# Kernel optimization log

Hardware: AMD Instinct MI355X
Metric: run time of the kernel (lower is better)

The kernel has to match this reference:

```python
import jax, jax.numpy as jnp
import numpy as np

N_HEADS = 16
EMBED = 1024
T = 2048        # given tokens
CACHE_NUM = 1024  # prepended cache tokens (x[0,-1] in the original)


def setup_inputs() -> dict:
    key = jax.random.key(0)
    k1, k2 = jax.random.split(key)
    qkv = jax.random.normal(k1, (T, 3 * EMBED), dtype=jnp.float32)
    # In the original these cache rows are torch.randn generated inside forward;
    # we lift them into a deterministic explicit input with identical semantics.
    cache = jax.random.normal(k2, (CACHE_NUM, 3 * EMBED), dtype=jnp.float32)
    return {"qkv": qkv, "cache": cache}


def reference(qkv, cache):
    C = EMBED
    H = N_HEADS
    D = C // H  # head_dim = 64
    t = qkv.shape[0]
    tc = cache.shape[0]
    t_full = t + tc  # T_ in the original

    gq, gk, gv = jnp.split(qkv, 3, axis=1)      # each [T, C]
    cq, ck, cv = jnp.split(cache, 3, axis=1)    # each [cache_num, C]

    q = jnp.concatenate([cq, gq], axis=0)  # [T_, C]
    k = jnp.concatenate([ck, gk], axis=0)
    v = jnp.concatenate([cv, gv], axis=0)

    # [T_, C] -> [H, T_, D]
    q = q.reshape(t_full, H, D).transpose(1, 0, 2)
    k = k.reshape(t_full, H, D).transpose(1, 0, 2)
    v = v.reshape(t_full, H, D).transpose(1, 0, 2)

    scale = 1.0 / np.sqrt(D).astype(np.float32)
    att = jnp.einsum('htd,hsd->hts', q, k) * scale  # [H, T_, T_]

    causal = jnp.tril(jnp.ones((t_full, t_full), dtype=bool))
    att = jnp.where(causal[None, :, :], att, jnp.float32(-jnp.inf))
    att = jax.nn.softmax(att, axis=-1)
    # attn_dropout is identity in eval / p=0

    y = jnp.einsum('hts,hsd->htd', att, v)          # [H, T_, D]
    y = y.transpose(1, 0, 2).reshape(t_full, C)     # [T_, C]
    return y[tc:, :]                                # drop cache rows -> [T, C]
```

## Files before the change

### kernel.cpp

```cpp
#include <hip/hip_runtime.h>
#include <cmath>


typedef _Float16 f16;
typedef __attribute__((ext_vector_type(8))) _Float16 f16x8;
typedef __attribute__((ext_vector_type(4))) _Float16 f16x4;
typedef __attribute__((ext_vector_type(2))) _Float16 f16x2;
typedef __attribute__((ext_vector_type(4))) float    f32x4;

constexpr int TC  = 1024;
constexpr int C3  = 3072;
constexpr int CE  = 1024;
constexpr int NH  = 16;
constexpr int TQ  = 2048;
constexpr int NKT = 48;

constexpr size_t KV_ELEMS = (size_t)NH * NKT * 4096;

constexpr int SPLITS[16] = {2,2,3,3,3,3,4,4,4,4,5,5,5,5,6,6};
constexpr int PRE[16]    = {0,2,4,7,10,13,16,20,24,28,32,37,42,47,52,58};
constexpr int NSLOT      = 64;

constexpr size_t OPART_E = (size_t)NSLOT * NH * 128 * 64;
constexpr size_t LPART_F = (size_t)NSLOT * NH * 128;

__device__ __forceinline__ void dma16(const void* g, void* l) {
    __builtin_amdgcn_global_load_lds(
        (const __attribute__((address_space(1))) void*)g,
        (__attribute__((address_space(3))) void*)l, 16, 0, 0);
}

__device__ __forceinline__ f16x2 pkrtz(float a, float b) {
    return __builtin_bit_cast(f16x2, __builtin_amdgcn_cvt_pkrtz(a, b));
}

__device__ __forceinline__ float fexp2(float x) {
    return __builtin_amdgcn_exp2f(x);
}

__global__ __launch_bounds__(256)
void prepass_f16(const float* __restrict__ qkv, const float* __restrict__ cache,
                 f16* __restrict__ Kt, f16* __restrict__ Vt)
{
    const int b   = blockIdx.x;
    const int xcd = b & 7;
    const int j   = b >> 3;
    const int h   = xcd * 2 + ((j >= 48) ? 1 : 0);
    const int kt  = (j >= 48) ? (j - 48) : j;

    const int tid = threadIdx.x;
    const int bt  = kt * 64;
    const float* src = (bt < TC) ? (cache + (size_t)bt * C3)
                                 : (qkv + (size_t)(bt - TC) * C3);
    f16* ktile = Kt + (size_t)(h * NKT + kt) * 4096;
    f16* vtile = Vt + (size_t)(h * NKT + kt) * 4096;

    __shared__ f16 vtmp[64 * 66];

    {
        const int tok = tid >> 2;
        const int c4  = tid & 3;
        const float* p = src + (size_t)tok * C3 + h * 64 + CE + c4 * 16;
        f32x4 x0 = ((const f32x4*)p)[0], x1 = ((const f32x4*)p)[1];
        f32x4 x2 = ((const f32x4*)p)[2], x3 = ((const f32x4*)p)[3];
        const int ch0 = (2 * c4)     ^ (tok & 7);
        const int ch1 = (2 * c4 + 1) ^ (tok & 7);
        *(f16x8*)&ktile[tok * 64 + ch0 * 8] =
            (f16x8){(f16)x0.x,(f16)x0.y,(f16)x0.z,(f16)x0.w,
                    (f16)x1.x,(f16)x1.y,(f16)x1.z,(f16)x1.w};
        *(f16x8*)&ktile[tok * 64 + ch1 * 8] =
            (f16x8){(f16)x2.x,(f16)x2.y,(f16)x2.z,(f16)x2.w,
                    (f16)x3.x,(f16)x3.y,(f16)x3.z,(f16)x3.w};
    }
    {
        const int tok  = tid >> 2;
        const int dblk = (tid & 3) * 16;
        const float* p = src + (size_t)tok * C3 + h * 64 + 2 * CE + dblk;
        f32x4 x0 = ((const f32x4*)p)[0], x1 = ((const f32x4*)p)[1];
        f32x4 x2 = ((const f32x4*)p)[2], x3 = ((const f32x4*)p)[3];
        float v[16] = {x0.x,x0.y,x0.z,x0.w, x1.x,x1.y,x1.z,x1.w,
                       x2.x,x2.y,x2.z,x2.w, x3.x,x3.y,x3.z,x3.w};
        f16* dst = &vtmp[tok * 66 + dblk];
        #pragma unroll
        for (int i = 0; i < 8; ++i)
            *(f16x2*)&dst[2 * i] = (f16x2){(f16)v[2 * i], (f16)v[2 * i + 1]};
    }
    __syncthreads();
    {
        const int d  = tid >> 2;
        const int oq = tid & 3;
        const int qd = oq ^ (d & 3);
        const int d4 = (d >> 2) & 1;
        f16 col[16];
        #pragma unroll
        for (int e = 0; e < 2; ++e)
            #pragma unroll
            for (int bb = 0; bb < 2; ++bb) {
                const int t0 = ((e ^ d4) * 2 + bb) * 16 + qd * 4;
                #pragma unroll
                for (int j = 0; j < 4; ++j)
                    col[e * 8 + bb * 4 + j] = vtmp[(t0 + j) * 66 + d];
            }
        *(f16x8*)&vtile[d * 64 + oq * 16] =
            (f16x8){col[0],col[1],col[2],col[3],col[4],col[5],col[6],col[7]};
        *(f16x8*)&vtile[d * 64 + oq * 16 + 8] =
            (f16x8){col[8],col[9],col[10],col[11],col[12],col[13],col[14],col[15]};
    }
}

__device__ __forceinline__ void tile_loop(
    const char* kg, const char* vg, int t0, int t1, int qbase_w,
    int l15, int quad, int ksw, int soff,
    const f16x8 (&qfrag)[2][2], f16 (&sKV)[2][8192],
    f32x4 (&o_accT)[2][4], float (&l_i)[2])
{
    {
        char* kl = (char*)&sKV[0][0]    + soff;
        char* vl = (char*)&sKV[0][4096] + soff;
        dma16(kg, kl);           dma16(kg + 1024, kl + 1024);
        dma16(vg, vl);           dma16(vg + 1024, vl + 1024);
    }
    int cur = 0;

    const int sA = ((quad ^ (l15 & 3)) << 1) + ((l15 >> 2) & 1);

    for (int kt = t0; kt < t1; ++kt) {
        asm volatile("s_waitcnt vmcnt(0) lgkmcnt(0)" ::: "memory");
        __syncthreads();

        kg += 8192; vg += 8192;
        if (kt + 1 < t1) {
            char* kl = (char*)&sKV[cur ^ 1][0]    + soff;
            char* vl = (char*)&sKV[cur ^ 1][4096] + soff;
            dma16(kg, kl);       dma16(kg + 1024, kl + 1024);
            dma16(vg, vl);       dma16(vg + 1024, vl + 1024);
        }
        const f16* sK  = &sKV[cur][0];
        const f16* sVT = &sKV[cur][4096];
        cur ^= 1;

        f32x4 sacc[2][4];
        #pragma unroll
        for (int u = 0; u < 2; ++u)
            #pragma unroll
            for (int kb = 0; kb < 4; ++kb) sacc[u][kb] = (f32x4){0.f,0.f,0.f,0.f};
        #pragma unroll
        for (int kb = 0; kb < 4; ++kb) {
            const int ib = (kb * 16 + l15) * 64 + ksw;
            f16x8 a0 = *(const f16x8*)&sK[ib];
            f16x8 a1 = *(const f16x8*)&sK[ib ^ 32];
            #pragma unroll
            for (int u = 0; u < 2; ++u) {
                sacc[u][kb] = __builtin_amdgcn_mfma_f32_16x16x32_f16(a0, qfrag[u][0], sacc[u][kb], 0, 0, 0);
                sacc[u][kb] = __builtin_amdgcn_mfma_f32_16x16x32_f16(a1, qfrag[u][1], sacc[u][kb], 0, 0, 0);
            }
        }

        if (kt * 64 + 63 > qbase_w) {
            #pragma unroll
            for (int u = 0; u < 2; ++u) {
                const int qg = qbase_w + u * 16 + l15;
                #pragma unroll
                for (int kb = 0; kb < 4; ++kb) {
                    const int kq = kt * 64 + kb * 16 + quad * 4;
                    #pragma unroll
                    for (int r = 0; r < 4; ++r)
                        if (kq + r > qg) sacc[u][kb][r] = -INFINITY;
                }
            }
        }

        f16x4 pfrag[2][4];
        #pragma unroll
        for (int u = 0; u < 2; ++u) {
            float ls = 0.f;
            #pragma unroll
            for (int kb = 0; kb < 4; ++kb) {
                const float p0 = fexp2(sacc[u][kb][0]);
                const float p1 = fexp2(sacc[u][kb][1]);
                const float p2 = fexp2(sacc[u][kb][2]);
                const float p3 = fexp2(sacc[u][kb][3]);
                ls += (p0 + p1) + (p2 + p3);
                f16x2 lo = pkrtz(p0, p1);
                f16x2 hi = pkrtz(p2, p3);
                pfrag[u][kb] = __builtin_shufflevector(lo, hi, 0, 1, 2, 3);
            }
            l_i[u] += ls;
        }

        #pragma unroll
        for (int dblk = 0; dblk < 4; ++dblk) {
            const int row = dblk * 16 + l15;
            f16x8 vv01 = *(const f16x8*)&sVT[row * 64 + sA * 8];
            f16x8 vv23 = *(const f16x8*)&sVT[row * 64 + (sA ^ 1) * 8];
            f16x4 vf[4];
            vf[0] = __builtin_shufflevector(vv01, vv01, 0, 1, 2, 3);
            vf[1] = __builtin_shufflevector(vv01, vv01, 4, 5, 6, 7);
            vf[2] = __builtin_shufflevector(vv23, vv23, 0, 1, 2, 3);
            vf[3] = __builtin_shufflevector(vv23, vv23, 4, 5, 6, 7);
            #pragma unroll
            for (int kb = 0; kb < 4; ++kb)
                #pragma unroll
                for (int u = 0; u < 2; ++u)
                    o_accT[u][dblk] = __builtin_amdgcn_mfma_f32_16x16x16f16(
                        vf[kb], pfrag[u][kb], o_accT[u][dblk], 0, 0, 0);
        }
    }
}

__global__ __launch_bounds__(256, 4)
void attn_splitk(const float* __restrict__ qkv,
                 const f16* __restrict__ Kt,
                 const f16* __restrict__ Vt,
                 f16*  __restrict__ Opart,
                 float* __restrict__ lpart)
{
    const int bb = blockIdx.x;
    const int xcd = bb & 7;
    const int j   = bb >> 3;
    const int h   = xcd * 2 + (j >> 6);
    const int g   = j & 63;
    int qt = 0;
    #pragma unroll
    for (int i = 1; i < 16; ++i) qt += (g >= PRE[i]) ? 1 : 0;
    const int s   = g - PRE[qt];
    const int nsp = SPLITS[qt];
    const int nkt = 2 * qt + 18;
    const int t0  = nkt * s / nsp;
    const int t1  = nkt * (s + 1) / nsp;

    const int tid  = threadIdx.x;
    const int w    = tid >> 6;
    const int lane = tid & 63;
    const int l15  = lane & 15;
    const int quad = lane >> 4;

    __shared__ __align__(16) f16 sKV[2][8192];

    const float qs = 0.125f * 1.44269504088896f;
    f16x8 qfrag[2][2];
    #pragma unroll
    for (int u = 0; u < 2; ++u) {
        const float* qp = qkv + (size_t)(qt * 128 + w * 32 + u * 16 + l15) * C3
                              + h * 64 + quad * 8;
        #pragma unroll
        for (int c = 0; c < 2; ++c) {
            f32x4 a = *(const f32x4*)(qp + c * 32);
            f32x4 b = *(const f32x4*)(qp + c * 32 + 4);
            qfrag[u][c] = (f16x8){(f16)(a.x * qs), (f16)(a.y * qs),
                                  (f16)(a.z * qs), (f16)(a.w * qs),
                                  (f16)(b.x * qs), (f16)(b.y * qs),
                                  (f16)(b.z * qs), (f16)(b.w * qs)};
        }
    }

    f32x4 o_accT[2][4];
    #pragma unroll
    for (int u = 0; u < 2; ++u)
        #pragma unroll
        for (int d = 0; d < 4; ++d) o_accT[u][d] = (f32x4){0.f, 0.f, 0.f, 0.f};
    float l_i[2] = {0.f, 0.f};

    const int qbase_w = TC + qt * 128 + w * 32;
    const int soff = w * 2048 + lane * 16;
    const char* kg = (const char*)(Kt + (size_t)(h * NKT + t0) * 4096) + soff;
    const char* vg = (const char*)(Vt + (size_t)(h * NKT + t0) * 4096) + soff;
    const int ksw = (quad ^ (l15 & 7)) * 8;

    tile_loop(kg, vg, t0, t1, qbase_w, l15, quad, ksw, soff,
              qfrag, sKV, o_accT, l_i);

    #pragma unroll
    for (int u = 0; u < 2; ++u) {
        float lf = l_i[u];
        lf += __shfl_xor(lf, 16);
        lf += __shfl_xor(lf, 32);
        const int qloc = w * 32 + u * 16 + l15;
        const int slot = PRE[qt] + s;
        f16*   op = Opart + ((size_t)slot * NH + h) * (128 * 64);
        float* lp = lpart + ((size_t)slot * NH + h) * 128;
        #pragma unroll
        for (int dblk = 0; dblk < 4; ++dblk) {
            f32x4 o = o_accT[u][dblk];
            f16x2 lo = pkrtz(o.x, o.y);
            f16x2 hi = pkrtz(o.z, o.w);
            *(f16x4*)&op[qloc * 64 + dblk * 16 + quad * 4] =
                __builtin_shufflevector(lo, hi, 0, 1, 2, 3);
        }
        if (quad == 0) lp[qloc] = lf;
    }
}

__global__ __launch_bounds__(256)
void attn_direct(const float* __restrict__ qkv,
                 const f16* __restrict__ Kt,
                 const f16* __restrict__ Vt,
                 float* __restrict__ out)
{
    const int bb  = blockIdx.x;
    const int h   = bb & 15;
    const int idx = bb >> 4;
    const int qt  = (h < 8) ? idx : 15 - idx;
    const int nsp = SPLITS[qt];
    const int nkt = 2 * qt + 18;

    const int tid  = threadIdx.x;
    const int w    = tid >> 6;
    const int lane = tid & 63;
    const int l15  = lane & 15;
    const int quad = lane >> 4;

    __shared__ __align__(16) f16 sKV[2][8192];

    const float qs = 0.125f * 1.44269504088896f;
    f16x8 qfrag[2][2];
    #pragma unroll
    for (int u = 0; u < 2; ++u) {
        const float* qp = qkv + (size_t)(qt * 128 + w * 32 + u * 16 + l15) * C3
                              + h * 64 + quad * 8;
        #pragma unroll
        for (int c = 0; c < 2; ++c) {
            f32x4 a = *(const f32x4*)(qp + c * 32);
            f32x4 b = *(const f32x4*)(qp + c * 32 + 4);
            qfrag[u][c] = (f16x8){(f16)(a.x * qs), (f16)(a.y * qs),
                                  (f16)(a.z * qs), (f16)(a.w * qs),
                                  (f16)(b.x * qs), (f16)(b.y * qs),
                                  (f16)(b.z * qs), (f16)(b.w * qs)};
        }
    }

    const int qbase_w = TC + qt * 128 + w * 32;
    const int soff = w * 2048 + lane * 16;
    const char* kg0 = (const char*)(Kt + (size_t)h * NKT * 4096) + soff;
    const char* vg0 = (const char*)(Vt + (size_t)h * NKT * 4096) + soff;
    const int ksw = (quad ^ (l15 & 7)) * 8;

    f32x4 osum[2][4];
    #pragma unroll
    for (int u = 0; u < 2; ++u)
        #pragma unroll
        for (int d = 0; d < 4; ++d) osum[u][d] = (f32x4){0.f, 0.f, 0.f, 0.f};
    float lsum[2] = {0.f, 0.f};

    for (int s = 0; s < nsp; ++s) {
        if (s) __syncthreads();
        const int t0 = nkt * s / nsp;
        const int t1 = nkt * (s + 1) / nsp;

        f32x4 o_accT[2][4];
        #pragma unroll
        for (int u = 0; u < 2; ++u)
            #pragma unroll
            for (int d = 0; d < 4; ++d) o_accT[u][d] = (f32x4){0.f,0.f,0.f,0.f};
        float l_i[2] = {0.f, 0.f};

        tile_loop(kg0 + (size_t)t0 * 8192, vg0 + (size_t)t0 * 8192,
                  t0, t1, qbase_w, l15, quad, ksw, soff,
                  qfrag, sKV, o_accT, l_i);

        #pragma unroll
        for (int u = 0; u < 2; ++u) {
            float lf = l_i[u];
            lf += __shfl_xor(lf, 16);
            lf += __shfl_xor(lf, 32);
            lsum[u] += lf;
            #pragma unroll
            for (int dblk = 0; dblk < 4; ++dblk) {
                f32x4 o = o_accT[u][dblk];
                f16x2 lo = pkrtz(o.x, o.y);
                f16x2 hi = pkrtz(o.z, o.w);
                osum[u][dblk].x += (float)lo[0];
                osum[u][dblk].y += (float)lo[1];
                osum[u][dblk].z += (float)hi[0];
                osum[u][dblk].w += (float)hi[1];
            }
        }
    }

    #pragma unroll
    for (int u = 0; u < 2; ++u) {
        const float inv = 1.0f / lsum[u];
        const int qloc = w * 32 + u * 16 + l15;
        const int gq = qt * 128 + qloc;
        #pragma unroll
        for (int dblk = 0; dblk < 4; ++dblk) {
            f32x4 o = osum[u][dblk];
            *(f32x4*)&out[(size_t)gq * CE + h * 64 + dblk * 16 + quad * 4] =
                (f32x4){o.x * inv, o.y * inv, o.z * inv, o.w * inv};
        }
    }
}

__global__ __launch_bounds__(256)
void combine_splits(const f16* __restrict__ Opart,
                    const float* __restrict__ lpart,
                    float* __restrict__ out)
{
    const int t  = blockIdx.x * 256 + threadIdx.x;
    const int d4 = t & 15;
    const int q  = (t >> 4) & (TQ - 1);
    const int h  = t >> 15;

    const int qt    = q >> 7;
    const int qloc  = q & 127;
    const int nsp   = SPLITS[qt];
    const int slot0 = PRE[qt];

    float lsum = 0.f;
    f32x4 acc = (f32x4){0.f, 0.f, 0.f, 0.f};
    for (int s = 0; s < nsp; ++s) {
        const size_t sb = (size_t)(slot0 + s) * NH + h;
        lsum += lpart[sb * 128 + qloc];
        f16x4 o = *(const f16x4*)&Opart[sb * (128 * 64) + qloc * 64 + d4 * 4];
        acc.x += (float)o[0]; acc.y += (float)o[1];
        acc.z += (float)o[2]; acc.w += (float)o[3];
    }
    const float inv = 1.0f / lsum;
    *(f32x4*)&out[(size_t)q * CE + h * 64 + d4 * 4] =
        (f32x4){acc.x * inv, acc.y * inv, acc.z * inv, acc.w * inv};
}

extern "C" void kernel_launch(void* const* d_in, const int* in_sizes, int n_in,
                              void* d_out, int out_size, void* d_ws, size_t ws_size,
                              hipStream_t stream)
{
    const float* qkv   = (const float*)d_in[0];
    const float* cache = (const float*)d_in[1];
    float*       out   = (float*)d_out;
    (void)in_sizes; (void)n_in; (void)out_size;

    const size_t kv_bytes = 2 * KV_ELEMS * sizeof(f16);
    const size_t need     = kv_bytes + OPART_E * sizeof(f16)
                          + LPART_F * sizeof(float);

    f16*   Kt    = (f16*)d_ws;
    f16*   Vt    = Kt + KV_ELEMS;
    f16*   Opart = (f16*)((char*)d_ws + kv_bytes);
    float* lpart = (float*)((char*)Opart + OPART_E * sizeof(f16));

    const int split = (ws_size >= need) ? 1 : 0;

    prepass_f16<<<dim3(NH * NKT), dim3(256), 0, stream>>>(qkv, cache, Kt, Vt);
    if (split) {
        attn_splitk<<<dim3(1024), dim3(256), 0, stream>>>(qkv, Kt, Vt, Opart, lpart);
        combine_splits<<<dim3(NH * TQ * 16 / 256), dim3(256), 0, stream>>>(
            Opart, lpart, out);
    } else {
        attn_direct<<<dim3(256), dim3(256), 0, stream>>>(qkv, Kt, Vt, out);
    }
}
```

Baseline: 112.7 us.

## Fuse prepass, split-K attention and combine into one cooperative kernel

```diff
diff --git a/kernel.cpp b/kernel.cpp
--- a/kernel.cpp
+++ b/kernel.cpp
@@ -1,5 +1,8 @@
 #include <hip/hip_runtime.h>
+#include <hip/hip_cooperative_groups.h>
 #include <cmath>
+
+namespace cg = cooperative_groups;
 
 
 typedef _Float16 f16;
@@ -38,24 +41,21 @@
     return __builtin_amdgcn_exp2f(x);
 }
 
-__global__ __launch_bounds__(256)
-void prepass_f16(const float* __restrict__ qkv, const float* __restrict__ cache,
-                 f16* __restrict__ Kt, f16* __restrict__ Vt)
-{
-    const int b   = blockIdx.x;
+__device__ __forceinline__ void prepass_body(
+    int b, int tid, const float* __restrict__ qkv,
+    const float* __restrict__ cache, f16* __restrict__ Kt,
+    f16* __restrict__ Vt, f16* vtmp)
+{
     const int xcd = b & 7;
     const int j   = b >> 3;
     const int h   = xcd * 2 + ((j >= 48) ? 1 : 0);
     const int kt  = (j >= 48) ? (j - 48) : j;
 
-    const int tid = threadIdx.x;
     const int bt  = kt * 64;
     const float* src = (bt < TC) ? (cache + (size_t)bt * C3)
                                  : (qkv + (size_t)(bt - TC) * C3);
     f16* ktile = Kt + (size_t)(h * NKT + kt) * 4096;
     f16* vtile = Vt + (size_t)(h * NKT + kt) * 4096;
-
-    __shared__ f16 vtmp[64 * 66];
 
     {
         const int tok = tid >> 2;
@@ -95,11 +95,11 @@
         #pragma unroll
         for (int e = 0; e < 2; ++e)
             #pragma unroll
-            for (int bb = 0; bb < 2; ++bb) {
-                const int t0 = ((e ^ d4) * 2 + bb) * 16 + qd * 4;
+            for (int bb2 = 0; bb2 < 2; ++bb2) {
+                const int t0 = ((e ^ d4) * 2 + bb2) * 16 + qd * 4;
                 #pragma unroll
-                for (int j = 0; j < 4; ++j)
-                    col[e * 8 + bb * 4 + j] = vtmp[(t0 + j) * 66 + d];
+                for (int jj = 0; jj < 4; ++jj)
+                    col[e * 8 + bb2 * 4 + jj] = vtmp[(t0 + jj) * 66 + d];
             }
         *(f16x8*)&vtile[d * 64 + oq * 16] =
             (f16x8){col[0],col[1],col[2],col[3],col[4],col[5],col[6],col[7]};
@@ -208,14 +208,11 @@
     }
 }
 
-__global__ __launch_bounds__(256, 4)
-void attn_splitk(const float* __restrict__ qkv,
-                 const f16* __restrict__ Kt,
-                 const f16* __restrict__ Vt,
-                 f16*  __restrict__ Opart,
-                 float* __restrict__ lpart)
-{
-    const int bb = blockIdx.x;
+__device__ __forceinline__ void attn_sk_body(
+    int bb, const float* __restrict__ qkv, const f16* __restrict__ Kt,
+    const f16* __restrict__ Vt, f16* __restrict__ Opart,
+    float* __restrict__ lpart, f16 (&sKV)[2][8192])
+{
     const int xcd = bb & 7;
     const int j   = bb >> 3;
     const int h   = xcd * 2 + (j >> 6);
@@ -234,8 +231,6 @@
     const int lane = tid & 63;
     const int l15  = lane & 15;
     const int quad = lane >> 4;
-
-    __shared__ __align__(16) f16 sKV[2][8192];
 
     const float qs = 0.125f * 1.44269504088896f;
     f16x8 qfrag[2][2];
@@ -289,6 +284,81 @@
         }
         if (quad == 0) lp[qloc] = lf;
     }
+}
+
+__device__ __forceinline__ void combine_unit(
+    int t, const f16* __restrict__ Opart, const float* __restrict__ lpart,
+    float* __restrict__ out)
+{
+    const int d4 = t & 15;
+    const int q  = (t >> 4) & (TQ - 1);
+    const int h  = t >> 15;
+
+    const int qt    = q >> 7;
+    const int qloc  = q & 127;
+    const int nsp   = SPLITS[qt];
+    const int slot0 = PRE[qt];
+
+    float lsum = 0.f;
+    f32x4 acc = (f32x4){0.f, 0.f, 0.f, 0.f};
+    for (int s = 0; s < nsp; ++s) {
+        const size_t sb = (size_t)(slot0 + s) * NH + h;
+        lsum += lpart[sb * 128 + qloc];
+        f16x4 o = *(const f16x4*)&Opart[sb * (128 * 64) + qloc * 64 + d4 * 4];
+        acc.x += (float)o[0]; acc.y += (float)o[1];
+        acc.z += (float)o[2]; acc.w += (float)o[3];
+    }
+    const float inv = 1.0f / lsum;
+    *(f32x4*)&out[(size_t)q * CE + h * 64 + d4 * 4] =
+        (f32x4){acc.x * inv, acc.y * inv, acc.z * inv, acc.w * inv};
+}
+
+__global__ __launch_bounds__(256, 4)
+void fused_all(const float* __restrict__ qkv, const float* __restrict__ cache,
+               f16* __restrict__ Kt, f16* __restrict__ Vt,
+               f16* __restrict__ Opart, float* __restrict__ lpart,
+               float* __restrict__ out)
+{
+    __shared__ __align__(16) f16 sKV[2][8192];
+    const int tid = threadIdx.x;
+
+    if (blockIdx.x < NH * NKT)
+        prepass_body(blockIdx.x, tid, qkv, cache, Kt, Vt, &sKV[0][0]);
+    cg::this_grid().sync();
+
+    attn_sk_body(blockIdx.x, qkv, Kt, Vt, Opart, lpart, sKV);
+    cg::this_grid().sync();
+
+    #pragma unroll
+    for (int k2 = 0; k2 < 2; ++k2)
+        combine_unit(blockIdx.x * 512 + k2 * 256 + tid, Opart, lpart, out);
+}
+
+__global__ __launch_bounds__(256)
+void prepass_f16(const float* __restrict__ qkv, const float* __restrict__ cache,
+                 f16* __restrict__ Kt, f16* __restrict__ Vt)
+{
+    __shared__ f16 vtmp[64 * 66];
+    prepass_body(blockIdx.x, threadIdx.x, qkv, cache, Kt, Vt, vtmp);
+}
+
+__global__ __launch_bounds__(256, 4)
+void attn_splitk(const float* __restrict__ qkv,
+                 const f16* __restrict__ Kt,
+                 const f16* __restrict__ Vt,
+                 f16*  __restrict__ Opart,
+                 float* __restrict__ lpart)
+{
+    __shared__ __align__(16) f16 sKV[2][8192];
+    attn_sk_body(blockIdx.x, qkv, Kt, Vt, Opart, lpart, sKV);
+}
+
+__global__ __launch_bounds__(256)
+void combine_splits(const f16* __restrict__ Opart,
+                    const float* __restrict__ lpart,
+                    float* __restrict__ out)
+{
+    combine_unit(blockIdx.x * 256 + threadIdx.x, Opart, lpart, out);
 }
 
 __global__ __launch_bounds__(256)
@@ -391,35 +461,6 @@
     }
 }
 
-__global__ __launch_bounds__(256)
-void combine_splits(const f16* __restrict__ Opart,
-                    const float* __restrict__ lpart,
-                    float* __restrict__ out)
-{
-    const int t  = blockIdx.x * 256 + threadIdx.x;
-    const int d4 = t & 15;
-    const int q  = (t >> 4) & (TQ - 1);
-    const int h  = t >> 15;
-
-    const int qt    = q >> 7;
-    const int qloc  = q & 127;
-    const int nsp   = SPLITS[qt];
-    const int slot0 = PRE[qt];
-
-    float lsum = 0.f;
-    f32x4 acc = (f32x4){0.f, 0.f, 0.f, 0.f};
-    for (int s = 0; s < nsp; ++s) {
-        const size_t sb = (size_t)(slot0 + s) * NH + h;
-        lsum += lpart[sb * 128 + qloc];
-        f16x4 o = *(const f16x4*)&Opart[sb * (128 * 64) + qloc * 64 + d4 * 4];
-        acc.x += (float)o[0]; acc.y += (float)o[1];
-        acc.z += (float)o[2]; acc.w += (float)o[3];
-    }
-    const float inv = 1.0f / lsum;
-    *(f32x4*)&out[(size_t)q * CE + h * 64 + d4 * 4] =
-        (f32x4){acc.x * inv, acc.y * inv, acc.z * inv, acc.w * inv};
-}
-
 extern "C" void kernel_launch(void* const* d_in, const int* in_sizes, int n_in,
                               void* d_out, int out_size, void* d_ws, size_t ws_size,
                               hipStream_t stream)
@@ -440,12 +481,26 @@
 
     const int split = (ws_size >= need) ? 1 : 0;
 
-    prepass_f16<<<dim3(NH * NKT), dim3(256), 0, stream>>>(qkv, cache, Kt, Vt);
     if (split) {
-        attn_splitk<<<dim3(1024), dim3(256), 0, stream>>>(qkv, Kt, Vt, Opart, lpart);
-        combine_splits<<<dim3(NH * TQ * 16 / 256), dim3(256), 0, stream>>>(
-            Opart, lpart, out);
+        int nb = 0;
+        hipError_t e = hipOccupancyMaxActiveBlocksPerMultiprocessor(
+            &nb, fused_all, 256, 0);
+        if (e == hipSuccess && nb >= 4) {
+            void* args[] = {(void*)&qkv, (void*)&cache, (void*)&Kt, (void*)&Vt,
+                            (void*)&Opart, (void*)&lpart, (void*)&out};
+            hipLaunchCooperativeKernel(fused_all, dim3(1024), dim3(256),
+                                       args, 0, stream);
+        } else {
+            prepass_f16<<<dim3(NH * NKT), dim3(256), 0, stream>>>(
+                qkv, cache, Kt, Vt);
+            attn_splitk<<<dim3(1024), dim3(256), 0, stream>>>(
+                qkv, Kt, Vt, Opart, lpart);
+            combine_splits<<<dim3(NH * TQ * 16 / 256), dim3(256), 0, stream>>>(
+                Opart, lpart, out);
+        }
     } else {
+        prepass_f16<<<dim3(NH * NKT), dim3(256), 0, stream>>>(
+            qkv, cache, Kt, Vt);
         attn_direct<<<dim3(256), dim3(256), 0, stream>>>(qkv, Kt, Vt, out);
     }
 }
```

Result: no change. 112.7 us (-0.1%).

## Load K/V fragments directly from global into registers, drop LDS staging

Applied to the files above, without the earlier changes.

```diff
diff --git a/kernel.cpp b/kernel.cpp
--- a/kernel.cpp
+++ b/kernel.cpp
@@ -24,12 +24,6 @@
 constexpr size_t OPART_E = (size_t)NSLOT * NH * 128 * 64;
 constexpr size_t LPART_F = (size_t)NSLOT * NH * 128;
 
-__device__ __forceinline__ void dma16(const void* g, void* l) {
-    __builtin_amdgcn_global_load_lds(
-        (const __attribute__((address_space(1))) void*)g,
-        (__attribute__((address_space(3))) void*)l, 16, 0, 0);
-}
-
 __device__ __forceinline__ f16x2 pkrtz(float a, float b) {
     return __builtin_bit_cast(f16x2, __builtin_amdgcn_cvt_pkrtz(a, b));
 }
@@ -63,12 +57,14 @@
         const float* p = src + (size_t)tok * C3 + h * 64 + CE + c4 * 16;
         f32x4 x0 = ((const f32x4*)p)[0], x1 = ((const f32x4*)p)[1];
         f32x4 x2 = ((const f32x4*)p)[2], x3 = ((const f32x4*)p)[3];
-        const int ch0 = (2 * c4)     ^ (tok & 7);
-        const int ch1 = (2 * c4 + 1) ^ (tok & 7);
-        *(f16x8*)&ktile[tok * 64 + ch0 * 8] =
+        const int kb  = tok >> 4;
+        const int l15 = tok & 15;
+        const int h2  = c4 >> 1;
+        const size_t base = kb * 1024 + h2 * 512 + (c4 & 1) * 256 + l15 * 8;
+        *(f16x8*)&ktile[base] =
             (f16x8){(f16)x0.x,(f16)x0.y,(f16)x0.z,(f16)x0.w,
                     (f16)x1.x,(f16)x1.y,(f16)x1.z,(f16)x1.w};
-        *(f16x8*)&ktile[tok * 64 + ch1 * 8] =
+        *(f16x8*)&ktile[base + 128] =
             (f16x8){(f16)x2.x,(f16)x2.y,(f16)x2.z,(f16)x2.w,
                     (f16)x3.x,(f16)x3.y,(f16)x3.z,(f16)x3.w};
     }
@@ -87,57 +83,46 @@
     }
     __syncthreads();
     {
-        const int d  = tid >> 2;
-        const int oq = tid & 3;
-        const int qd = oq ^ (d & 3);
-        const int d4 = (d >> 2) & 1;
-        f16 col[16];
-        #pragma unroll
-        for (int e = 0; e < 2; ++e)
-            #pragma unroll
-            for (int bb = 0; bb < 2; ++bb) {
-                const int t0 = ((e ^ d4) * 2 + bb) * 16 + qd * 4;
+        const int d    = tid >> 2;
+        const int qd   = tid & 3;
+        const int dblk = d >> 4;
+        const int dl   = d & 15;
+        #pragma unroll
+        for (int kp = 0; kp < 2; ++kp) {
+            f16 col[8];
+            #pragma unroll
+            for (int bb = 0; bb < 2; ++bb)
                 #pragma unroll
-                for (int j = 0; j < 4; ++j)
-                    col[e * 8 + bb * 4 + j] = vtmp[(t0 + j) * 66 + d];
-            }
-        *(f16x8*)&vtile[d * 64 + oq * 16] =
-            (f16x8){col[0],col[1],col[2],col[3],col[4],col[5],col[6],col[7]};
-        *(f16x8*)&vtile[d * 64 + oq * 16 + 8] =
-            (f16x8){col[8],col[9],col[10],col[11],col[12],col[13],col[14],col[15]};
+                for (int jj = 0; jj < 4; ++jj)
+                    col[bb * 4 + jj] =
+                        vtmp[((2 * kp + bb) * 16 + qd * 4 + jj) * 66 + d];
+            *(f16x8*)&vtile[dblk * 1024 + kp * 512 + (qd * 16 + dl) * 8] =
+                (f16x8){col[0],col[1],col[2],col[3],
+                        col[4],col[5],col[6],col[7]};
+        }
     }
 }
 
 __device__ __forceinline__ void tile_loop(
-    const char* kg, const char* vg, int t0, int t1, int qbase_w,
-    int l15, int quad, int ksw, int soff,
-    const f16x8 (&qfrag)[2][2], f16 (&sKV)[2][8192],
+    const char* kt_p, const char* vt_p, int t0, int t1, int qbase_w,
+    int l15, int quad,
+    const f16x8 (&qfrag)[2][2],
     f32x4 (&o_accT)[2][4], float (&l_i)[2])
 {
-    {
-        char* kl = (char*)&sKV[0][0]    + soff;
-        char* vl = (char*)&sKV[0][4096] + soff;
-        dma16(kg, kl);           dma16(kg + 1024, kl + 1024);
-        dma16(vg, vl);           dma16(vg + 1024, vl + 1024);
-    }
-    int cur = 0;
-
-    const int sA = ((quad ^ (l15 & 3)) << 1) + ((l15 >> 2) & 1);
-
     for (int kt = t0; kt < t1; ++kt) {
-        asm volatile("s_waitcnt vmcnt(0) lgkmcnt(0)" ::: "memory");
-        __syncthreads();
-
-        kg += 8192; vg += 8192;
-        if (kt + 1 < t1) {
-            char* kl = (char*)&sKV[cur ^ 1][0]    + soff;
-            char* vl = (char*)&sKV[cur ^ 1][4096] + soff;
-            dma16(kg, kl);       dma16(kg + 1024, kl + 1024);
-            dma16(vg, vl);       dma16(vg + 1024, vl + 1024);
-        }
-        const f16* sK  = &sKV[cur][0];
-        const f16* sVT = &sKV[cur][4096];
-        cur ^= 1;
+        f16x8 ka[4][2];
+        f16x8 vv[4][2];
+        #pragma unroll
+        for (int kb = 0; kb < 4; ++kb) {
+            ka[kb][0] = *(const f16x8*)(kt_p + kb * 2048);
+            ka[kb][1] = *(const f16x8*)(kt_p + kb * 2048 + 1024);
+        }
+        #pragma unroll
+        for (int db = 0; db < 4; ++db) {
+            vv[db][0] = *(const f16x8*)(vt_p + db * 2048);
+            vv[db][1] = *(const f16x8*)(vt_p + db * 2048 + 1024);
+        }
+        kt_p += 8192; vt_p += 8192;
 
         f32x4 sacc[2][4];
         #pragma unroll
@@ -146,13 +131,10 @@
             for (int kb = 0; kb < 4; ++kb) sacc[u][kb] = (f32x4){0.f,0.f,0.f,0.f};
         #pragma unroll
         for (int kb = 0; kb < 4; ++kb) {
-            const int ib = (kb * 16 + l15) * 64 + ksw;
-            f16x8 a0 = *(const f16x8*)&sK[ib];
-            f16x8 a1 = *(const f16x8*)&sK[ib ^ 32];
             #pragma unroll
             for (int u = 0; u < 2; ++u) {
-                sacc[u][kb] = __builtin_amdgcn_mfma_f32_16x16x32_f16(a0, qfrag[u][0], sacc[u][kb], 0, 0, 0);
-                sacc[u][kb] = __builtin_amdgcn_mfma_f32_16x16x32_f16(a1, qfrag[u][1], sacc[u][kb], 0, 0, 0);
+                sacc[u][kb] = __builtin_amdgcn_mfma_f32_16x16x32_f16(ka[kb][0], qfrag[u][0], sacc[u][kb], 0, 0, 0);
+                sacc[u][kb] = __builtin_amdgcn_mfma_f32_16x16x32_f16(ka[kb][1], qfrag[u][1], sacc[u][kb], 0, 0, 0);
             }
         }
 
@@ -190,14 +172,11 @@
 
         #pragma unroll
         for (int dblk = 0; dblk < 4; ++dblk) {
-            const int row = dblk * 16 + l15;
-            f16x8 vv01 = *(const f16x8*)&sVT[row * 64 + sA * 8];
-            f16x8 vv23 = *(const f16x8*)&sVT[row * 64 + (sA ^ 1) * 8];
             f16x4 vf[4];
-            vf[0] = __builtin_shufflevector(vv01, vv01, 0, 1, 2, 3);
-            vf[1] = __builtin_shufflevector(vv01, vv01, 4, 5, 6, 7);
-            vf[2] = __builtin_shufflevector(vv23, vv23, 0, 1, 2, 3);
-            vf[3] = __builtin_shufflevector(vv23, vv23, 4, 5, 6, 7);
+            vf[0] = __builtin_shufflevector(vv[dblk][0], vv[dblk][0], 0, 1, 2, 3);
+            vf[1] = __builtin_shufflevector(vv[dblk][0], vv[dblk][0], 4, 5, 6, 7);
+            vf[2] = __builtin_shufflevector(vv[dblk][1], vv[dblk][1], 0, 1, 2, 3);
+            vf[3] = __builtin_shufflevector(vv[dblk][1], vv[dblk][1], 4, 5, 6, 7);
             #pragma unroll
             for (int kb = 0; kb < 4; ++kb)
                 #pragma unroll
@@ -208,7 +187,7 @@
     }
 }
 
-__global__ __launch_bounds__(256, 4)
+__global__ __launch_bounds__(256, 3)
 void attn_splitk(const float* __restrict__ qkv,
                  const f16* __restrict__ Kt,
                  const f16* __restrict__ Vt,
@@ -234,8 +213,6 @@
     const int lane = tid & 63;
     const int l15  = lane & 15;
     const int quad = lane >> 4;
-
-    __shared__ __align__(16) f16 sKV[2][8192];
 
     const float qs = 0.125f * 1.44269504088896f;
     f16x8 qfrag[2][2];
@@ -262,13 +239,12 @@
     float l_i[2] = {0.f, 0.f};
 
     const int qbase_w = TC + qt * 128 + w * 32;
-    const int soff = w * 2048 + lane * 16;
-    const char* kg = (const char*)(Kt + (size_t)(h * NKT + t0) * 4096) + soff;
-    const char* vg = (const char*)(Vt + (size_t)(h * NKT + t0) * 4096) + soff;
-    const int ksw = (quad ^ (l15 & 7)) * 8;
-
-    tile_loop(kg, vg, t0, t1, qbase_w, l15, quad, ksw, soff,
-              qfrag, sKV, o_accT, l_i);
+    const char* kt_p = (const char*)(Kt + (size_t)(h * NKT + t0) * 4096)
+                     + lane * 16;
+    const char* vt_p = (const char*)(Vt + (size_t)(h * NKT + t0) * 4096)
+                     + lane * 16;
+
+    tile_loop(kt_p, vt_p, t0, t1, qbase_w, l15, quad, qfrag, o_accT, l_i);
 
     #pragma unroll
     for (int u = 0; u < 2; ++u) {
@@ -291,7 +267,7 @@
     }
 }
 
-__global__ __launch_bounds__(256)
+__global__ __launch_bounds__(256, 3)
 void attn_direct(const float* __restrict__ qkv,
                  const f16* __restrict__ Kt,
                  const f16* __restrict__ Vt,
@@ -309,8 +285,6 @@
     const int lane = tid & 63;
     const int l15  = lane & 15;
     const int quad = lane >> 4;
-
-    __shared__ __align__(16) f16 sKV[2][8192];
 
     const float qs = 0.125f * 1.44269504088896f;
     f16x8 qfrag[2][2];
@@ -330,10 +304,8 @@
     }
 
     const int qbase_w = TC + qt * 128 + w * 32;
-    const int soff = w * 2048 + lane * 16;
-    const char* kg0 = (const char*)(Kt + (size_t)h * NKT * 4096) + soff;
-    const char* vg0 = (const char*)(Vt + (size_t)h * NKT * 4096) + soff;
-    const int ksw = (quad ^ (l15 & 7)) * 8;
+    const char* kg0 = (const char*)(Kt + (size_t)h * NKT * 4096) + lane * 16;
+    const char* vg0 = (const char*)(Vt + (size_t)h * NKT * 4096) + lane * 16;
 
     f32x4 osum[2][4];
     #pragma unroll
@@ -343,7 +315,6 @@
     float lsum[2] = {0.f, 0.f};
 
     for (int s = 0; s < nsp; ++s) {
-        if (s) __syncthreads();
         const int t0 = nkt * s / nsp;
         const int t1 = nkt * (s + 1) / nsp;
 
@@ -355,8 +326,7 @@
         float l_i[2] = {0.f, 0.f};
 
         tile_loop(kg0 + (size_t)t0 * 8192, vg0 + (size_t)t0 * 8192,
-                  t0, t1, qbase_w, l15, quad, ksw, soff,
-                  qfrag, sKV, o_accT, l_i);
+                  t0, t1, qbase_w, l15, quad, qfrag, o_accT, l_i);
 
         #pragma unroll
         for (int u = 0; u < 2; ++u) {
```

Result: slower. 118.5 us (+5.1%).

## Pair query tiles per 512-thread block sharing K/V tiles with uniform 8-way split

Applied to the files above, without the earlier changes.

```diff
diff --git a/kernel.cpp b/kernel.cpp
--- a/kernel.cpp
+++ b/kernel.cpp
@@ -17,12 +17,10 @@
 
 constexpr size_t KV_ELEMS = (size_t)NH * NKT * 4096;
 
-constexpr int SPLITS[16] = {2,2,3,3,3,3,4,4,4,4,5,5,5,5,6,6};
-constexpr int PRE[16]    = {0,2,4,7,10,13,16,20,24,28,32,37,42,47,52,58};
-constexpr int NSLOT      = 64;
-
-constexpr size_t OPART_E = (size_t)NSLOT * NH * 128 * 64;
-constexpr size_t LPART_F = (size_t)NSLOT * NH * 128;
+constexpr int NSLOT = 64;
+
+constexpr size_t OPART_E = (size_t)NSLOT * NH * 256 * 64;
+constexpr size_t LPART_F = (size_t)NSLOT * NH * 256;
 
 __device__ __forceinline__ void dma16(const void* g, void* l) {
     __builtin_amdgcn_global_load_lds(
@@ -95,11 +93,11 @@
         #pragma unroll
         for (int e = 0; e < 2; ++e)
             #pragma unroll
-            for (int bb = 0; bb < 2; ++bb) {
-                const int t0 = ((e ^ d4) * 2 + bb) * 16 + qd * 4;
+            for (int bb2 = 0; bb2 < 2; ++bb2) {
+                const int t0 = ((e ^ d4) * 2 + bb2) * 16 + qd * 4;
                 #pragma unroll
-                for (int j = 0; j < 4; ++j)
-                    col[e * 8 + bb * 4 + j] = vtmp[(t0 + j) * 66 + d];
+                for (int jj = 0; jj < 4; ++jj)
+                    col[e * 8 + bb2 * 4 + jj] = vtmp[(t0 + jj) * 66 + d];
             }
         *(f16x8*)&vtile[d * 64 + oq * 16] =
             (f16x8){col[0],col[1],col[2],col[3],col[4],col[5],col[6],col[7]};
@@ -108,6 +106,7 @@
     }
 }
 
+template<int NDMA>
 __device__ __forceinline__ void tile_loop(
     const char* kg, const char* vg, int t0, int t1, int qbase_w,
     int l15, int quad, int ksw, int soff,
@@ -117,8 +116,11 @@
     {
         char* kl = (char*)&sKV[0][0]    + soff;
         char* vl = (char*)&sKV[0][4096] + soff;
-        dma16(kg, kl);           dma16(kg + 1024, kl + 1024);
-        dma16(vg, vl);           dma16(vg + 1024, vl + 1024);
+        #pragma unroll
+        for (int i2 = 0; i2 < NDMA; ++i2) {
+            dma16(kg + i2 * 1024, kl + i2 * 1024);
+            dma16(vg + i2 * 1024, vl + i2 * 1024);
+        }
     }
     int cur = 0;
 
@@ -132,8 +134,11 @@
         if (kt + 1 < t1) {
             char* kl = (char*)&sKV[cur ^ 1][0]    + soff;
             char* vl = (char*)&sKV[cur ^ 1][4096] + soff;
-            dma16(kg, kl);       dma16(kg + 1024, kl + 1024);
-            dma16(vg, vl);       dma16(vg + 1024, vl + 1024);
+            #pragma unroll
+            for (int i2 = 0; i2 < NDMA; ++i2) {
+                dma16(kg + i2 * 1024, kl + i2 * 1024);
+                dma16(vg + i2 * 1024, vl + i2 * 1024);
+            }
         }
         const f16* sK  = &sKV[cur][0];
         const f16* sVT = &sKV[cur][4096];
@@ -208,7 +213,7 @@
     }
 }
 
-__global__ __launch_bounds__(256, 4)
+__global__ __launch_bounds__(512, 8)
 void attn_splitk(const float* __restrict__ qkv,
                  const f16* __restrict__ Kt,
                  const f16* __restrict__ Vt,
@@ -220,20 +225,19 @@
     const int j   = bb >> 3;
     const int h   = xcd * 2 + (j >> 6);
     const int g   = j & 63;
-    int qt = 0;
-    #pragma unroll
-    for (int i = 1; i < 16; ++i) qt += (g >= PRE[i]) ? 1 : 0;
-    const int s   = g - PRE[qt];
-    const int nsp = SPLITS[qt];
-    const int nkt = 2 * qt + 18;
-    const int t0  = nkt * s / nsp;
-    const int t1  = nkt * (s + 1) / nsp;
+    const int pair = g >> 3;
+    const int s    = g & 7;
+    const int nkt_u = 4 * pair + 20;
+    const int t0  = nkt_u * s / 8;
+    const int t1  = nkt_u * (s + 1) / 8;
 
     const int tid  = threadIdx.x;
     const int w    = tid >> 6;
     const int lane = tid & 63;
     const int l15  = lane & 15;
     const int quad = lane >> 4;
+    const int qt   = pair * 2 + (w >> 2);
+    const int wloc = w & 3;
 
     __shared__ __align__(16) f16 sKV[2][8192];
 
@@ -241,8 +245,9 @@
     f16x8 qfrag[2][2];
     #pragma unroll
     for (int u = 0; u < 2; ++u) {
-        const float* qp = qkv + (size_t)(qt * 128 + w * 32 + u * 16 + l15) * C3
-                              + h * 64 + quad * 8;
+        const float* qp = qkv
+            + (size_t)(qt * 128 + wloc * 32 + u * 16 + l15) * C3
+            + h * 64 + quad * 8;
         #pragma unroll
         for (int c = 0; c < 2; ++c) {
             f32x4 a = *(const f32x4*)(qp + c * 32);
@@ -261,24 +266,24 @@
         for (int d = 0; d < 4; ++d) o_accT[u][d] = (f32x4){0.f, 0.f, 0.f, 0.f};
     float l_i[2] = {0.f, 0.f};
 
-    const int qbase_w = TC + qt * 128 + w * 32;
-    const int soff = w * 2048 + lane * 16;
+    const int qbase_w = TC + qt * 128 + wloc * 32;
+    const int soff = w * 1024 + lane * 16;
     const char* kg = (const char*)(Kt + (size_t)(h * NKT + t0) * 4096) + soff;
     const char* vg = (const char*)(Vt + (size_t)(h * NKT + t0) * 4096) + soff;
     const int ksw = (quad ^ (l15 & 7)) * 8;
 
-    tile_loop(kg, vg, t0, t1, qbase_w, l15, quad, ksw, soff,
-              qfrag, sKV, o_accT, l_i);
-
+    tile_loop<1>(kg, vg, t0, t1, qbase_w, l15, quad, ksw, soff,
+                 qfrag, sKV, o_accT, l_i);
+
+    const int slot = pair * 8 + s;
+    f16*   op = Opart + ((size_t)slot * NH + h) * (256 * 64);
+    float* lp = lpart + ((size_t)slot * NH + h) * 256;
     #pragma unroll
     for (int u = 0; u < 2; ++u) {
         float lf = l_i[u];
         lf += __shfl_xor(lf, 16);
         lf += __shfl_xor(lf, 32);
-        const int qloc = w * 32 + u * 16 + l15;
-        const int slot = PRE[qt] + s;
-        f16*   op = Opart + ((size_t)slot * NH + h) * (128 * 64);
-        float* lp = lpart + ((size_t)slot * NH + h) * 128;
+        const int qloc = (w >> 2) * 128 + wloc * 32 + u * 16 + l15;
         #pragma unroll
         for (int dblk = 0; dblk < 4; ++dblk) {
             f32x4 o = o_accT[u][dblk];
@@ -301,8 +306,8 @@
     const int h   = bb & 15;
     const int idx = bb >> 4;
     const int qt  = (h < 8) ? idx : 15 - idx;
-    const int nsp = SPLITS[qt];
-    const int nkt = 2 * qt + 18;
+    const int pair  = qt >> 1;
+    const int nkt_u = 4 * pair + 20;
 
     const int tid  = threadIdx.x;
     const int w    = tid >> 6;
@@ -342,10 +347,10 @@
         for (int d = 0; d < 4; ++d) osum[u][d] = (f32x4){0.f, 0.f, 0.f, 0.f};
     float lsum[2] = {0.f, 0.f};
 
-    for (int s = 0; s < nsp; ++s) {
+    for (int s = 0; s < 8; ++s) {
         if (s) __syncthreads();
-        const int t0 = nkt * s / nsp;
-        const int t1 = nkt * (s + 1) / nsp;
+        const int t0 = nkt_u * s / 8;
+        const int t1 = nkt_u * (s + 1) / 8;
 
         f32x4 o_accT[2][4];
         #pragma unroll
@@ -354,9 +359,9 @@
             for (int d = 0; d < 4; ++d) o_accT[u][d] = (f32x4){0.f,0.f,0.f,0.f};
         float l_i[2] = {0.f, 0.f};
 
-        tile_loop(kg0 + (size_t)t0 * 8192, vg0 + (size_t)t0 * 8192,
-                  t0, t1, qbase_w, l15, quad, ksw, soff,
-                  qfrag, sKV, o_accT, l_i);
+        tile_loop<2>(kg0 + (size_t)t0 * 8192, vg0 + (size_t)t0 * 8192,
+                     t0, t1, qbase_w, l15, quad, ksw, soff,
+                     qfrag, sKV, o_accT, l_i);
 
         #pragma unroll
         for (int u = 0; u < 2; ++u) {
@@ -402,16 +407,17 @@
     const int h  = t >> 15;
 
     const int qt    = q >> 7;
-    const int qloc  = q & 127;
-    const int nsp   = SPLITS[qt];
-    const int slot0 = PRE[qt];
+    const int pair  = qt >> 1;
+    const int qr    = ((qt & 1) << 7) + (q & 127);
+    const int slot0 = pair * 8;
 
     float lsum = 0.f;
     f32x4 acc = (f32x4){0.f, 0.f, 0.f, 0.f};
-    for (int s = 0; s < nsp; ++s) {
+    #pragma unroll
+    for (int s = 0; s < 8; ++s) {
         const size_t sb = (size_t)(slot0 + s) * NH + h;
-        lsum += lpart[sb * 128 + qloc];
-        f16x4 o = *(const f16x4*)&Opart[sb * (128 * 64) + qloc * 64 + d4 * 4];
+        lsum += lpart[sb * 256 + qr];
+        f16x4 o = *(const f16x4*)&Opart[sb * (256 * 64) + qr * 64 + d4 * 4];
         acc.x += (float)o[0]; acc.y += (float)o[1];
         acc.z += (float)o[2]; acc.w += (float)o[3];
     }
@@ -442,7 +448,8 @@
 
     prepass_f16<<<dim3(NH * NKT), dim3(256), 0, stream>>>(qkv, cache, Kt, Vt);
     if (split) {
-        attn_splitk<<<dim3(1024), dim3(256), 0, stream>>>(qkv, Kt, Vt, Opart, lpart);
+        attn_splitk<<<dim3(1024), dim3(512), 0, stream>>>(
+            qkv, Kt, Vt, Opart, lpart);
         combine_splits<<<dim3(NH * TQ * 16 / 256), dim3(256), 0, stream>>>(
             Opart, lpart, out);
     } else {
```

Measured after the change: 255.0 us. 126% more time.
